# Kernel tuning notes

Hardware: AMD Instinct MI355X
Metric: run time of the kernel (lower is better)

The kernel has to match this reference:

```python
import jax, jax.numpy as jnp
import numpy as np

ALPHA = 0.2  # LeakyReLU negative slope
NEG_INF = -9e15  # mask value used by the original module


def setup_inputs() -> dict:
    key = jax.random.key(0)
    k1, k2, k3, k4 = jax.random.split(key, 4)
    B, N, F_in, F_out = 8, 2048, 128, 64
    h = jax.random.normal(k1, (B, N, F_in), dtype=jnp.float32)
    adj = jax.random.randint(k2, (B, N, N), 0, 2, dtype=jnp.int32)
    # xavier_uniform with gain=1.414
    def xavier(k, shape, gain=1.414):
        fan_in, fan_out = shape[0], shape[1]
        bound = gain * np.sqrt(6.0 / (fan_in + fan_out))
        return jax.random.uniform(k, shape, jnp.float32, -bound, bound)
    W = xavier(k3, (F_in, F_out))
    a = xavier(k4, (2 * F_out, 1))
    return {"h": h, "adj": adj, "W": W, "a": a}


def reference(h, adj, W, a):
    # h: [B,N,F_in], adj: [B,N,N], W: [F_in,F_out], a: [2*F_out,1]
    F_out = W.shape[1]
    Wh = jnp.matmul(h, W)                       # [B,N,F_out]
    # Rank-1 decomposition of the additive score: e_ij = leaky_relu(a1.Wh_i + a2.Wh_j)
    # (same math as cat([Wh_i, Wh_j]) @ a, without the O(N^2 * 2F) intermediate)
    a1 = a[:F_out, 0]
    a2 = a[F_out:, 0]
    s1 = jnp.einsum('bnf,f->bn', Wh, a1)        # scores for node i
    s2 = jnp.einsum('bnf,f->bn', Wh, a2)        # scores for node j
    e = jax.nn.leaky_relu(s1[:, :, None] + s2[:, None, :], negative_slope=ALPHA)  # [B,N,N]
    attention = jnp.where(adj > 0, e, jnp.float32(NEG_INF))
    attention = jax.nn.softmax(attention, axis=2)
    # dropout is identity in eval mode
    h_out = jnp.matmul(attention, Wh)           # [B,N,F_out]
    return jax.nn.elu(h_out), attention
```

## Files before the change

### kernel.cpp

```cpp
#include <hip/hip_runtime.h>

#define GAT_ALPHA 0.2f
#define INV_N (1.0f / 2048.0f)

typedef float f32x4 __attribute__((ext_vector_type(4)));
typedef __bf16 bf16x8 __attribute__((ext_vector_type(8)));
typedef unsigned short us8 __attribute__((ext_vector_type(8)));
typedef unsigned short us4 __attribute__((ext_vector_type(4)));

__device__ __forceinline__ unsigned short f2bf(float x) {
  union { float f; unsigned u; } v; v.f = x;
  unsigned r = v.u + 0x7FFFu + ((v.u >> 16) & 1u);
  return (unsigned short)(r >> 16);
}
__device__ __forceinline__ float lrelu(float x) {
  return fmaxf(x, 0.f) + GAT_ALPHA * fminf(x, 0.f);
}
__device__ __forceinline__ void lgkm_barrier() {
  asm volatile("s_waitcnt lgkmcnt(0)" ::: "memory");
  __builtin_amdgcn_s_barrier();
  __builtin_amdgcn_sched_barrier(0);
}

__global__ __launch_bounds__(256)
void k0_wh(const float* __restrict__ h, const float* __restrict__ W,
           const float* __restrict__ a, unsigned short* __restrict__ WhT,
           float* __restrict__ s1g, float* __restrict__ s2g)
{
  __shared__ float h_s[64][132];
  __shared__ float W_s[128][64];
  __shared__ float wt_s[64][66];
  __shared__ float a_s[128];
  const int t = threadIdx.x;
  const int b = blockIdx.y;
  const int r0 = blockIdx.x * 64;

#pragma unroll
  for (int v = 0; v < 8; ++v) {
    int c = v * 256 + t;
    int k = c >> 4, fo = (c & 15) << 2;
    *(float4*)&W_s[k][fo] = *(const float4*)&W[k * 64 + fo];
  }
#pragma unroll
  for (int v = 0; v < 8; ++v) {
    int c = v * 256 + t;
    int r = c >> 5, ko = (c & 31) << 2;
    *(float4*)&h_s[r][ko] = *(const float4*)&h[((size_t)(b * 2048 + r0 + r)) * 128 + ko];
  }
  if (t < 128) a_s[t] = a[t];
  __syncthreads();

  const int tg = t >> 4;
  const int tf = (t & 15) << 2;
  float acc[4][4] = {};
#pragma unroll
  for (int k4 = 0; k4 < 32; ++k4) {
    float4 hv[4];
#pragma unroll
    for (int i = 0; i < 4; ++i)
      hv[i] = *(const float4*)&h_s[i * 16 + tg][k4 * 4];
#pragma unroll
    for (int kk = 0; kk < 4; ++kk) {
      float4 wv = *(const float4*)&W_s[k4 * 4 + kk][tf];
#pragma unroll
      for (int i = 0; i < 4; ++i) {
        float hx = ((const float*)&hv[i])[kk];
        acc[i][0] = fmaf(hx, wv.x, acc[i][0]);
        acc[i][1] = fmaf(hx, wv.y, acc[i][1]);
        acc[i][2] = fmaf(hx, wv.z, acc[i][2]);
        acc[i][3] = fmaf(hx, wv.w, acc[i][3]);
      }
    }
  }
#pragma unroll
  for (int i = 0; i < 4; ++i)
#pragma unroll
    for (int j = 0; j < 4; ++j)
      wt_s[tf + j][i * 16 + tg] = acc[i][j];
  __syncthreads();

  if (t < 64) {
    float v1 = 0.f, v2 = 0.f;
#pragma unroll 8
    for (int f = 0; f < 64; ++f) {
      float w = wt_s[f][t];
      v1 = fmaf(w, a_s[f], v1);
      v2 = fmaf(w, a_s[64 + f], v2);
    }
    s1g[b * 2048 + r0 + t] = v1;
    s2g[b * 2048 + r0 + t] = v2;
  }
  {
    int f = t >> 2, rb = (t & 3) << 4;
    unsigned short pk[16];
#pragma unroll
    for (int i = 0; i < 16; ++i) pk[i] = f2bf(wt_s[f][rb + i]);
    size_t base = ((size_t)(b * 64 + f)) * 2048 + r0 + rb;
    *(uint4*)&WhT[base]     = *(uint4*)&pk[0];
    *(uint4*)&WhT[base + 8] = *(uint4*)&pk[8];
  }
}

__global__ __launch_bounds__(256)
void k1_stats(const int* __restrict__ adj, const float* __restrict__ s1g,
              const float* __restrict__ s2g, float* __restrict__ lrow,
              unsigned long long* __restrict__ gmask)
{
  const int t = threadIdx.x;
  const int l = t & 63, wv = t >> 6;
  const int i = blockIdx.x, b = blockIdx.y;
  const size_t row = (size_t)(b * 2048 + i);

  const int4 a0 = *(const int4*)&adj[row * 2048 + 4 * t];
  const int4 a1 = *(const int4*)&adj[row * 2048 + 1024 + 4 * t];
  const float4 z0 = *(const float4*)&s2g[b * 2048 + 4 * t];
  const float4 z1 = *(const float4*)&s2g[b * 2048 + 1024 + 4 * t];

  unsigned long long m00 = __ballot(a0.x > 0), m01 = __ballot(a0.y > 0);
  unsigned long long m02 = __ballot(a0.z > 0), m03 = __ballot(a0.w > 0);
  unsigned long long m10 = __ballot(a1.x > 0), m11 = __ballot(a1.y > 0);
  unsigned long long m12 = __ballot(a1.z > 0), m13 = __ballot(a1.w > 0);
  if (l == 0) {
    unsigned long long* g = gmask + row * 32;
    ulonglong2 p0; p0.x = m00; p0.y = m01;
    ulonglong2 p1; p1.x = m02; p1.y = m03;
    ulonglong2 p2; p2.x = m10; p2.y = m11;
    ulonglong2 p3; p3.x = m12; p3.y = m13;
    *(ulonglong2*)&g[wv * 4]          = p0;
    *(ulonglong2*)&g[wv * 4 + 2]      = p1;
    *(ulonglong2*)&g[16 + wv * 4]     = p2;
    *(ulonglong2*)&g[16 + wv * 4 + 2] = p3;
  }

  const float s1v = s1g[row];
  float sum = 0.f;
  sum += (a0.x > 0) ? __expf(lrelu(s1v + z0.x)) : 0.f;
  sum += (a0.y > 0) ? __expf(lrelu(s1v + z0.y)) : 0.f;
  sum += (a0.z > 0) ? __expf(lrelu(s1v + z0.z)) : 0.f;
  sum += (a0.w > 0) ? __expf(lrelu(s1v + z0.w)) : 0.f;
  sum += (a1.x > 0) ? __expf(lrelu(s1v + z1.x)) : 0.f;
  sum += (a1.y > 0) ? __expf(lrelu(s1v + z1.y)) : 0.f;
  sum += (a1.z > 0) ? __expf(lrelu(s1v + z1.z)) : 0.f;
  sum += (a1.w > 0) ? __expf(lrelu(s1v + z1.w)) : 0.f;
#pragma unroll
  for (int o = 32; o > 0; o >>= 1) sum += __shfl_xor(sum, o);
  __shared__ float red2[4];
  if (l == 0) red2[wv] = sum;
  __syncthreads();
  if (t == 0) lrow[row] = red2[0] + red2[1] + red2[2] + red2[3];
}

__global__ __launch_bounds__(256)
void k2_main(const unsigned long long* __restrict__ gmask,
             const unsigned short* __restrict__ WhT,
             const float* __restrict__ s1g, const float* __restrict__ s2g,
             const float* __restrict__ lrow,
             float* __restrict__ pp0, float* __restrict__ pp1,
             float* __restrict__ att)
{
  __shared__ unsigned short att_s[32][136];
  __shared__ unsigned short wh_s[64][136];
  __shared__ unsigned long long bm_s[32][16];
  __shared__ float s1_s[32], il_s[32];

  const int t = threadIdx.x;
  const int b = blockIdx.z;
  const int jh = blockIdx.y;
  const int jb = jh << 10;
  const int r0 = blockIdx.x * 32;
  const size_t rowb = (size_t)(b * 2048 + r0);

  {
    int rr = t >> 3, wq = (t & 7) << 1;
    ulonglong2 v = *(const ulonglong2*)&gmask[(rowb + rr) * 32 + jh * 16 + wq];
    bm_s[rr][wq] = v.x; bm_s[rr][wq + 1] = v.y;
  }
  if (t < 32) {
    float L = lrow[rowb + t];
    s1_s[t] = s1g[rowb + t];
    il_s[t] = (L > 0.f) ? 1.f / L : -1.f;
  }
  __syncthreads();

  const int w  = t >> 6, l = t & 63;
  const int rt  = (w & 1) << 4;
  const int ft0 = (w >> 1) << 1;
  const int ln = l & 15, lg = l >> 4;
  f32x4 acc0 = {0.f, 0.f, 0.f, 0.f};
  f32x4 acc1 = {0.f, 0.f, 0.f, 0.f};

  const int ff = t >> 4, ko = (t & 15) << 3;

  for (int j0 = jb; j0 < jb + 1024; j0 += 128) {
    uint4 wreg[4];
#pragma unroll
    for (int v = 0; v < 4; ++v)
      wreg[v] = *(const uint4*)&WhT[((size_t)(b * 64 + (v * 16 + ff))) * 2048 + j0 + ko];

#pragma unroll
    for (int it = 0; it < 4; ++it) {
      const int r  = (t >> 5) + (it << 3);
      const int jj = (t & 31) << 2;
      const int j  = j0 + jj;
      const float s1v = s1_s[r], il = il_s[r];
      const bool uni = (il < 0.f);
      const int lc4 = ((j >> 8) & 3) << 2;
      const int pos = (j & 255) >> 2;
      const unsigned long long w0 = bm_s[r][lc4 + 0];
      const unsigned long long w1 = bm_s[r][lc4 + 1];
      const unsigned long long w2 = bm_s[r][lc4 + 2];
      const unsigned long long w3 = bm_s[r][lc4 + 3];
      const float4 zv = *(const float4*)&s2g[b * 2048 + j];
      f32x4 o;
#define PW(dst, zz, wq)                                             \
      { float e = __expf(lrelu(s1v + (zz))) * il;                   \
        dst = uni ? INV_N : ((((wq) >> pos) & 1ull) ? e : 0.f); }
      PW(o[0], zv.x, w0) PW(o[1], zv.y, w1) PW(o[2], zv.z, w2) PW(o[3], zv.w, w3)
#undef PW
      __builtin_nontemporal_store(o, (f32x4*)&att[(rowb + r) * 2048 + j]);
      us4 pk;
      pk.x = f2bf(o[0]); pk.y = f2bf(o[1]); pk.z = f2bf(o[2]); pk.w = f2bf(o[3]);
      *(us4*)&att_s[r][jj] = pk;
    }
#pragma unroll
    for (int v = 0; v < 4; ++v)
      *(uint4*)&wh_s[v * 16 + ff][ko] = wreg[v];

    lgkm_barrier();
#pragma unroll
    for (int ks = 0; ks < 4; ++ks) {
      union { us8 u; bf16x8 v; } a0c, b0c, b1c;
      a0c.u = *(const us8*)&att_s[rt + ln][ks * 32 + lg * 8];
      b0c.u = *(const us8*)&wh_s[ft0 * 16 + ln][ks * 32 + lg * 8];
      b1c.u = *(const us8*)&wh_s[ft0 * 16 + 16 + ln][ks * 32 + lg * 8];
      acc0 = __builtin_amdgcn_mfma_f32_16x16x32_bf16(a0c.v, b0c.v, acc0, 0, 0, 0);
      acc1 = __builtin_amdgcn_mfma_f32_16x16x32_bf16(a0c.v, b1c.v, acc1, 0, 0, 0);
    }
    lgkm_barrier();
  }
  float* __restrict__ pp = (jh == 0) ? pp0 : pp1;
#pragma unroll
  for (int q = 0; q < 4; ++q) {
    int r = rt + lg * 4 + q;
    pp[(rowb + r) * 64 + ft0 * 16 + ln]       = acc0[q];
    pp[(rowb + r) * 64 + (ft0 + 1) * 16 + ln] = acc1[q];
  }
}

__global__ __launch_bounds__(256)
void k3_elu(const float* __restrict__ pp0, const float* __restrict__ pp1,
            float* __restrict__ hout)
{
  const size_t idx = ((size_t)blockIdx.x * 256 + threadIdx.x) * 4;
  float4 a = *(const float4*)&pp0[idx];
  float4 c = *(const float4*)&pp1[idx];
  float4 o;
  float x;
  x = a.x + c.x; o.x = (x > 0.f) ? x : expm1f(x);
  x = a.y + c.y; o.y = (x > 0.f) ? x : expm1f(x);
  x = a.z + c.z; o.z = (x > 0.f) ? x : expm1f(x);
  x = a.w + c.w; o.w = (x > 0.f) ? x : expm1f(x);
  *(float4*)&hout[idx] = o;
}

extern "C" void kernel_launch(void* const* d_in, const int* in_sizes, int n_in,
                              void* d_out, int out_size, void* d_ws, size_t ws_size,
                              hipStream_t stream)
{
  const float* h   = (const float*)d_in[0];
  const int*   adj = (const int*)d_in[1];
  const float* W   = (const float*)d_in[2];
  const float* a   = (const float*)d_in[3];
  float* hout = (float*)d_out;
  float* att  = hout + (size_t)8 * 2048 * 64;

  char* ws = (char*)d_ws;
  unsigned short* WhT = (unsigned short*)ws;
  float* s1 = (float*)(ws + (size_t)(2u << 20));
  float* s2 = s1 + 16384;
  float* lr = s2 + 16384;
  unsigned long long* gmask =
      (unsigned long long*)(ws + (size_t)(2u << 20) + 3 * 65536);
  float* pp0 = (float*)(ws + (size_t)(2u << 20) + 3 * 65536 + (4u << 20));
  float* pp1 = pp0 + (size_t)8 * 2048 * 64;

  k0_wh   <<<dim3(32, 8),    256, 0, stream>>>(h, W, a, WhT, s1, s2);
  k1_stats<<<dim3(2048, 8),  256, 0, stream>>>(adj, s1, s2, lr, gmask);
  k2_main <<<dim3(64, 2, 8), 256, 0, stream>>>(gmask, WhT, s1, s2, lr, pp0, pp1, att);
  k3_elu  <<<dim3(1024),     256, 0, stream>>>(pp0, pp1, hout);
}
```

Measured before the change: 72.88 us.

## Halve k2 row tile, give each wave its own Wh slice, double-buffer attention tile

The attention/PV kernel now handles 16 rows per block instead of 32, which doubles the grid. Each wave owns a private 16-feature slice of Wh in shared memory, and the bf16 attention tile is double-buffered. Together these remove the second block barrier in each j-iteration. The s2 vector load and the mask-index math are hoisted out of the row loop. The trade-off is that each block now reloads the full Wh chunk for half as many rows, doubling Wh reads through L2, in exchange for less synchronization stall and more parallelism.

```diff
diff --git a/kernel.cpp b/kernel.cpp
--- a/kernel.cpp
+++ b/kernel.cpp
@@ -151,31 +151,27 @@
 }
 
 __global__ __launch_bounds__(256)
-void k2_main(const unsigned long long* __restrict__ gmask,
-             const unsigned short* __restrict__ WhT,
-             const float* __restrict__ s1g, const float* __restrict__ s2g,
-             const float* __restrict__ lrow,
-             float* __restrict__ pp0, float* __restrict__ pp1,
-             float* __restrict__ att)
-{
-  __shared__ unsigned short att_s[32][136];
-  __shared__ unsigned short wh_s[64][136];
-  __shared__ unsigned long long bm_s[32][16];
-  __shared__ float s1_s[32], il_s[32];
+void k2_att_pv(const unsigned long long* __restrict__ gmask,
+               const unsigned short* __restrict__ WhT,
+               const float* __restrict__ s1g, const float* __restrict__ s2g,
+               const float* __restrict__ lrow,
+               float* __restrict__ pp0, float* __restrict__ pp1,
+               float* __restrict__ att)
+{
+  __shared__ unsigned long long bm_s[16][16];
+  __shared__ float s1_s[16], il_s[16];
+  __shared__ unsigned short att_s[2][16][136];
+  __shared__ unsigned short wh_s[4][16][136];
 
   const int t = threadIdx.x;
   const int b = blockIdx.z;
   const int jh = blockIdx.y;
   const int jb = jh << 10;
-  const int r0 = blockIdx.x * 32;
+  const int r0 = blockIdx.x * 16;
   const size_t rowb = (size_t)(b * 2048 + r0);
 
-  {
-    int rr = t >> 3, wq = (t & 7) << 1;
-    ulonglong2 v = *(const ulonglong2*)&gmask[(rowb + rr) * 32 + jh * 16 + wq];
-    bm_s[rr][wq] = v.x; bm_s[rr][wq + 1] = v.y;
-  }
-  if (t < 32) {
+  bm_s[t >> 4][t & 15] = gmask[(rowb + (t >> 4)) * 32 + jh * 16 + (t & 15)];
+  if (t < 16) {
     float L = lrow[rowb + t];
     s1_s[t] = s1g[rowb + t];
     il_s[t] = (L > 0.f) ? 1.f / L : -1.f;
@@ -183,67 +179,64 @@
   __syncthreads();
 
   const int w  = t >> 6, l = t & 63;
-  const int rt  = (w & 1) << 4;
-  const int ft0 = (w >> 1) << 1;
   const int ln = l & 15, lg = l >> 4;
-  f32x4 acc0 = {0.f, 0.f, 0.f, 0.f};
-  f32x4 acc1 = {0.f, 0.f, 0.f, 0.f};
-
-  const int ff = t >> 4, ko = (t & 15) << 3;
-
+  const int jj = (t & 31) << 2;
+  const int rbase = (t >> 5) & 7;
+  const unsigned short* __restrict__ wsrc =
+      WhT + ((size_t)(b * 64 + w * 16)) * 2048;
+  f32x4 acc = {0.f, 0.f, 0.f, 0.f};
+
+  int p = 0;
   for (int j0 = jb; j0 < jb + 1024; j0 += 128) {
     uint4 wreg[4];
 #pragma unroll
     for (int v = 0; v < 4; ++v)
-      wreg[v] = *(const uint4*)&WhT[((size_t)(b * 64 + (v * 16 + ff))) * 2048 + j0 + ko];
-
-#pragma unroll
-    for (int it = 0; it < 4; ++it) {
-      const int r  = (t >> 5) + (it << 3);
-      const int jj = (t & 31) << 2;
-      const int j  = j0 + jj;
-      const float s1v = s1_s[r], il = il_s[r];
+      wreg[v] = *(const uint4*)&wsrc[(size_t)(v * 4 + lg) * 2048 + j0 + ln * 8];
+
+    const int j = j0 + jj;
+    const float4 zv = *(const float4*)&s2g[b * 2048 + j];
+    const int lc4 = ((j >> 8) & 3) << 2;
+    const int pos = (j & 255) >> 2;
+#pragma unroll
+    for (int it = 0; it < 2; ++it) {
+      const int rr = rbase + (it << 3);
+      const float s1r = s1_s[rr], il = il_s[rr];
       const bool uni = (il < 0.f);
-      const int lc4 = ((j >> 8) & 3) << 2;
-      const int pos = (j & 255) >> 2;
-      const unsigned long long w0 = bm_s[r][lc4 + 0];
-      const unsigned long long w1 = bm_s[r][lc4 + 1];
-      const unsigned long long w2 = bm_s[r][lc4 + 2];
-      const unsigned long long w3 = bm_s[r][lc4 + 3];
-      const float4 zv = *(const float4*)&s2g[b * 2048 + j];
+      const unsigned long long w0 = bm_s[rr][lc4 + 0];
+      const unsigned long long w1 = bm_s[rr][lc4 + 1];
+      const unsigned long long w2 = bm_s[rr][lc4 + 2];
+      const unsigned long long w3 = bm_s[rr][lc4 + 3];
       f32x4 o;
 #define PW(dst, zz, wq)                                             \
-      { float e = __expf(lrelu(s1v + (zz))) * il;                   \
+      { float e = __expf(lrelu(s1r + (zz))) * il;                   \
         dst = uni ? INV_N : ((((wq) >> pos) & 1ull) ? e : 0.f); }
       PW(o[0], zv.x, w0) PW(o[1], zv.y, w1) PW(o[2], zv.z, w2) PW(o[3], zv.w, w3)
 #undef PW
-      __builtin_nontemporal_store(o, (f32x4*)&att[(rowb + r) * 2048 + j]);
+      __builtin_nontemporal_store(o, (f32x4*)&att[(rowb + rr) * 2048 + j]);
       us4 pk;
       pk.x = f2bf(o[0]); pk.y = f2bf(o[1]); pk.z = f2bf(o[2]); pk.w = f2bf(o[3]);
-      *(us4*)&att_s[r][jj] = pk;
+      *(us4*)&att_s[p][rr][jj] = pk;
     }
 #pragma unroll
     for (int v = 0; v < 4; ++v)
-      *(uint4*)&wh_s[v * 16 + ff][ko] = wreg[v];
+      *(uint4*)&wh_s[w][v * 4 + lg][ln * 8] = wreg[v];
 
     lgkm_barrier();
 #pragma unroll
     for (int ks = 0; ks < 4; ++ks) {
-      union { us8 u; bf16x8 v; } a0c, b0c, b1c;
-      a0c.u = *(const us8*)&att_s[rt + ln][ks * 32 + lg * 8];
-      b0c.u = *(const us8*)&wh_s[ft0 * 16 + ln][ks * 32 + lg * 8];
-      b1c.u = *(const us8*)&wh_s[ft0 * 16 + 16 + ln][ks * 32 + lg * 8];
-      acc0 = __builtin_amdgcn_mfma_f32_16x16x32_bf16(a0c.v, b0c.v, acc0, 0, 0, 0);
-      acc1 = __builtin_amdgcn_mfma_f32_16x16x32_bf16(a0c.v, b1c.v, acc1, 0, 0, 0);
-    }
-    lgkm_barrier();
-  }
+      union { us8 u; bf16x8 v; } ac, bc;
+      ac.u = *(const us8*)&att_s[p][ln][ks * 32 + lg * 8];
+      bc.u = *(const us8*)&wh_s[w][ln][ks * 32 + lg * 8];
+      acc = __builtin_amdgcn_mfma_f32_16x16x32_bf16(ac.v, bc.v, acc, 0, 0, 0);
+    }
+    p ^= 1;
+  }
+
   float* __restrict__ pp = (jh == 0) ? pp0 : pp1;
 #pragma unroll
   for (int q = 0; q < 4; ++q) {
-    int r = rt + lg * 4 + q;
-    pp[(rowb + r) * 64 + ft0 * 16 + ln]       = acc0[q];
-    pp[(rowb + r) * 64 + (ft0 + 1) * 16 + ln] = acc1[q];
+    const int rr = lg * 4 + q;
+    pp[(rowb + rr) * 64 + w * 16 + ln] = acc[q];
   }
 }
 
@@ -284,8 +277,8 @@
   float* pp0 = (float*)(ws + (size_t)(2u << 20) + 3 * 65536 + (4u << 20));
   float* pp1 = pp0 + (size_t)8 * 2048 * 64;
 
-  k0_wh   <<<dim3(32, 8),    256, 0, stream>>>(h, W, a, WhT, s1, s2);
-  k1_stats<<<dim3(2048, 8),  256, 0, stream>>>(adj, s1, s2, lr, gmask);
-  k2_main <<<dim3(64, 2, 8), 256, 0, stream>>>(gmask, WhT, s1, s2, lr, pp0, pp1, att);
-  k3_elu  <<<dim3(1024),     256, 0, stream>>>(pp0, pp1, hout);
-}
+  k0_wh    <<<dim3(32, 8),     256, 0, stream>>>(h, W, a, WhT, s1, s2);
+  k1_stats <<<dim3(2048, 8),   256, 0, stream>>>(adj, s1, s2, lr, gmask);
+  k2_att_pv<<<dim3(128, 2, 8), 256, 0, stream>>>(gmask, WhT, s1, s2, lr, pp0, pp1, att);
+  k3_elu   <<<dim3(1024),      256, 0, stream>>>(pp0, pp1, hout);
+}
```

Result: no change. 73.02 us, median of 2 (+0.2%).
